# Performance work log

Hardware: AMD Instinct MI355X
Metric: run time of the kernel (lower is better)

## Reference

```python
import jax, jax.numpy as jnp
import numpy as np

N_NODES = 100000
N_EDGES = 1600000
D_IN = 128
D_HID = 128
N_LAYERS = 3


def setup_inputs() -> dict:
    key = jax.random.key(0)
    ks = jax.random.split(key, 7)
    x = jax.random.normal(ks[0], (N_NODES, D_IN), dtype=jnp.float32)
    edge_index = jax.random.randint(ks[1], (2, N_EDGES), 0, N_NODES, dtype=jnp.int32)
    s = 1.0 / np.sqrt(D_HID)
    # stacked per-layer MLP params: lin1 (in->h), lin2 (h->h); in==h==128 for all layers
    W1 = jax.random.uniform(ks[2], (N_LAYERS, D_IN, D_HID), jnp.float32, -s, s)
    b1 = jax.random.uniform(ks[3], (N_LAYERS, D_HID), jnp.float32, -s, s)
    W2 = jax.random.uniform(ks[4], (N_LAYERS, D_HID, D_HID), jnp.float32, -s, s)
    b2 = jax.random.uniform(ks[5], (N_LAYERS, D_HID), jnp.float32, -s, s)
    return {"x": x, "edge_index": edge_index, "W1": W1, "b1": b1, "W2": W2, "b2": b2}


def _gin_layer(x, src, dst, W1, b1, W2, b2):
    # GINConv: out = MLP((1+eps)*x + sum_{j in N(i)} x_j), eps = 0
    agg = jax.ops.segment_sum(x[src], dst, num_segments=N_NODES)  # [N, C]
    h = x + agg
    h = jnp.maximum(h @ W1 + b1, 0.0)  # MLP internal ReLU
    return h @ W2 + b2


def reference(x, edge_index, W1, b1, W2, b2):
    src, dst = edge_index[0], edge_index[1]
    for i in range(N_LAYERS):
        x = _gin_layer(x, src, dst, W1[i], b1[i], W2[i], b2[i])
        if i < N_LAYERS - 1:  # inter-layer act (norm=Identity, dropout=0)
            x = jnp.maximum(x, 0.0)
    return x
```

## Files before the change

### kernel.cpp

```cpp
#include <hip/hip_runtime.h>
#include <hip/hip_bf16.h>

#define D 128

typedef float f32x4 __attribute__((ext_vector_type(4)));
typedef __bf16 bf16x8 __attribute__((ext_vector_type(8)));

__device__ __forceinline__ unsigned short f2bf(float f) {
  unsigned int u = __float_as_uint(f);
  u += 0x7fff + ((u >> 16) & 1);
  return (unsigned short)(u >> 16);
}

__device__ __forceinline__ void gl_lds16(const void* g, void* l) {
  __builtin_amdgcn_global_load_lds(
      (const __attribute__((address_space(1))) unsigned int*)g,
      (__attribute__((address_space(3))) unsigned int*)l, 16, 0, 0);
}


__global__ void k_hist(const int* __restrict__ dst, int E, int* __restrict__ deg) {
  int e = blockIdx.x * 256 + threadIdx.x;
  if (e < E) atomicAdd(&deg[dst[e]], 1);
}

__device__ __forceinline__ int wave_incl_scan(int v, int lane) {
#pragma unroll
  for (int d = 1; d < 64; d <<= 1) {
    int t = __shfl_up(v, d);
    if (lane >= d) v += t;
  }
  return v;
}

__global__ void k_bsum(const int* __restrict__ deg, int N, int* __restrict__ bsum) {
  int i = blockIdx.x * 256 + threadIdx.x;
  int v = (i < N) ? deg[i] : 0;
#pragma unroll
  for (int d = 32; d >= 1; d >>= 1) v += __shfl_down(v, d);
  __shared__ int ws[4];
  if ((threadIdx.x & 63) == 0) ws[threadIdx.x >> 6] = v;
  __syncthreads();
  if (threadIdx.x == 0) bsum[blockIdx.x] = ws[0] + ws[1] + ws[2] + ws[3];
}

__global__ void k_scanp(const int* __restrict__ bsum, int NB, int* __restrict__ bscan,
                        int* __restrict__ total_out) {
  int t = threadIdx.x;
  int lane = t & 63, w = t >> 6;
  int v = (t < NB) ? bsum[t] : 0;
  int s = wave_incl_scan(v, lane);
  __shared__ int ws[8];
  if (lane == 63) ws[w] = s;
  __syncthreads();
  int off = 0;
  for (int i = 0; i < w; i++) off += ws[i];
  if (t < NB) bscan[t] = off + s - v;
  if (t == 0) {
    int tot = 0;
    for (int i = 0; i < 8; i++) tot += ws[i];
    total_out[0] = tot;
  }
}

__global__ void k_scanf(const int* __restrict__ deg, int N, const int* __restrict__ bscan,
                        int* __restrict__ row_ptr) {
  int i = blockIdx.x * 256 + threadIdx.x;
  int lane = threadIdx.x & 63, w = threadIdx.x >> 6;
  int v = (i < N) ? deg[i] : 0;
  int s = wave_incl_scan(v, lane);
  __shared__ int ws[4];
  if (lane == 63) ws[w] = s;
  __syncthreads();
  int off = 0;
  for (int k = 0; k < w; k++) off += ws[k];
  if (i < N) row_ptr[i] = bscan[blockIdx.x] + off + s - v;
}

#define NBK 196
#define CHUNK 4096
__global__ __launch_bounds__(256) void k_binA(const int* __restrict__ src,
                                              const int* __restrict__ dst, int E,
                                              const int* __restrict__ row_ptr,
                                              int* __restrict__ bcursor,
                                              int* __restrict__ pairbuf) {
  __shared__ int cnt[NBK];
  __shared__ int base[NBK];
  const int tid = threadIdx.x;
  const int e0 = blockIdx.x * CHUNK;
  const int emax = min(e0 + CHUNK, E);
  for (int i = tid; i < NBK; i += 256) cnt[i] = 0;
  __syncthreads();
  for (int e = e0 + tid; e < emax; e += 256)
    atomicAdd(&cnt[((unsigned)dst[e]) >> 9], 1);
  __syncthreads();
  for (int i = tid; i < NBK; i += 256) {
    int c = cnt[i];
    int b = 0;
    if (c) b = atomicAdd(&bcursor[i], c) + row_ptr[i << 9];
    base[i] = b;
    cnt[i] = 0;
  }
  __syncthreads();
  for (int e = e0 + tid; e < emax; e += 256) {
    int d = dst[e];
    int bk = ((unsigned)d) >> 9;
    int pos = base[bk] + atomicAdd(&cnt[bk], 1);
    pairbuf[pos] = (src[e] << 9) | (d & 511);
  }
}

#define SEG_CAP 12800
__global__ __launch_bounds__(256) void k_binB(const int* __restrict__ pairbuf,
                                              const int* __restrict__ row_ptr,
                                              int* __restrict__ col, int N) {
  __shared__ int rp[513];
  __shared__ int cur[512];
  __shared__ int stage[SEG_CAP];
  const int tid = threadIdx.x;
  const int node0 = blockIdx.x << 9;
  const int nn = min(512, N - node0);
  for (int i = tid; i <= nn; i += 256) rp[i] = row_ptr[node0 + i];
  for (int i = tid; i < 512; i += 256) cur[i] = 0;
  __syncthreads();
  const int start = rp[0];
  const int sz = rp[nn] - start;
  for (int i = tid; i < sz; i += 256) {
    int pk = pairbuf[start + i];
    int d = pk & 511;
    int pos = (rp[d] - start) + atomicAdd(&cur[d], 1);
    if (pos < SEG_CAP) stage[pos] = (int)(((unsigned)pk) >> 9);
  }
  __syncthreads();
  for (int i = tid; i < sz; i += 256) col[start + i] = stage[i];
}

__global__ __launch_bounds__(256) void k_agg(const unsigned short* __restrict__ Y,
                                             const int* __restrict__ row_ptr,
                                             const int* __restrict__ col,
                                             const float* __restrict__ bias,
                                             unsigned short* __restrict__ H, int N) {
  int wid = (blockIdx.x * 256 + threadIdx.x) >> 6;
  int lane = threadIdx.x & 63;
  if (wid >= N) return;
  const unsigned int* Yu = (const unsigned int*)Y;
  unsigned int sv = Yu[(size_t)wid * 64 + lane];
  float2 bv = ((const float2*)bias)[lane];
  float ax = bv.x + __uint_as_float(sv << 16);
  float ay = bv.y + __uint_as_float(sv & 0xffff0000u);
  int rs = row_ptr[wid], re = row_ptr[wid + 1];
  int deg = re - rs;
  int dcap = min(deg, 64);
  int cv = (lane < dcap) ? col[rs + lane] : 0;
  int j = 0;
  for (; j + 8 <= dcap; j += 8) {
    int s0 = __shfl(cv, j + 0), s1 = __shfl(cv, j + 1);
    int s2 = __shfl(cv, j + 2), s3 = __shfl(cv, j + 3);
    int s4 = __shfl(cv, j + 4), s5 = __shfl(cv, j + 5);
    int s6 = __shfl(cv, j + 6), s7 = __shfl(cv, j + 7);
    unsigned int v0 = Yu[(size_t)s0 * 64 + lane];
    unsigned int v1 = Yu[(size_t)s1 * 64 + lane];
    unsigned int v2 = Yu[(size_t)s2 * 64 + lane];
    unsigned int v3 = Yu[(size_t)s3 * 64 + lane];
    unsigned int v4 = Yu[(size_t)s4 * 64 + lane];
    unsigned int v5 = Yu[(size_t)s5 * 64 + lane];
    unsigned int v6 = Yu[(size_t)s6 * 64 + lane];
    unsigned int v7 = Yu[(size_t)s7 * 64 + lane];
    ax += ((__uint_as_float(v0 << 16) + __uint_as_float(v1 << 16)) +
           (__uint_as_float(v2 << 16) + __uint_as_float(v3 << 16))) +
          ((__uint_as_float(v4 << 16) + __uint_as_float(v5 << 16)) +
           (__uint_as_float(v6 << 16) + __uint_as_float(v7 << 16)));
    ay += ((__uint_as_float(v0 & 0xffff0000u) + __uint_as_float(v1 & 0xffff0000u)) +
           (__uint_as_float(v2 & 0xffff0000u) + __uint_as_float(v3 & 0xffff0000u))) +
          ((__uint_as_float(v4 & 0xffff0000u) + __uint_as_float(v5 & 0xffff0000u)) +
           (__uint_as_float(v6 & 0xffff0000u) + __uint_as_float(v7 & 0xffff0000u)));
  }
  for (; j < dcap; j++) {
    int s = __shfl(cv, j);
    unsigned int v = Yu[(size_t)s * 64 + lane];
    ax += __uint_as_float(v << 16);
    ay += __uint_as_float(v & 0xffff0000u);
  }
  for (int t = rs + 64; t < re; t++) {
    unsigned int v = Yu[(size_t)col[t] * 64 + lane];
    ax += __uint_as_float(v << 16);
    ay += __uint_as_float(v & 0xffff0000u);
  }
  ax = fmaxf(ax, 0.f);
  ay = fmaxf(ay, 0.f);
  unsigned int packed = ((unsigned int)f2bf(ay) << 16) | f2bf(ax);
  ((unsigned int*)H)[(size_t)wid * 64 + lane] = packed;
}

__global__ void k_prep(const float* __restrict__ W1, const float* __restrict__ W2,
                       unsigned short* __restrict__ Wt) {
  int b = blockIdx.x;
  const float* W = (b & 1) ? (W2 + (size_t)(b >> 1) * D * D) : (W1 + (size_t)(b >> 1) * D * D);
  unsigned short* O = Wt + (size_t)b * D * D;
  for (int i = threadIdx.x; i < D * D; i += 256) {
    int n = i >> 7, k = i & 127;
    O[n * D + k] = f2bf(W[k * D + n]);
  }
}

template <bool A_FP32, bool OUT_FP32>
__global__ __launch_bounds__(256) void k_gemm(const void* __restrict__ Ain,
                                              const unsigned short* __restrict__ Wt,
                                              const float* __restrict__ bias,
                                              void* __restrict__ Cout, int M, int relu) {
  __shared__ __align__(16) unsigned short As[64 * 128];
  __shared__ __align__(16) unsigned short Bs[128 * 128];
  const int tid = threadIdx.x;
  const int wid = tid >> 6, lane = tid & 63;
  const int R0 = blockIdx.x * 64;

#pragma unroll
  for (int g = 0; g < 8; g++) {
    int flat = g * 256 + tid;
    int n = flat >> 4, p = flat & 15;
    int l = p ^ (n & 15);
    gl_lds16(Wt + (size_t)n * D + l * 8, &Bs[(size_t)(g * 256 + wid * 64) * 8]);
  }
  if (A_FP32) {
    const float* A = (const float*)Ain;
#pragma unroll
    for (int g = 0; g < 4; g++) {
      int flat = g * 256 + tid;
      int row = flat >> 4, p = flat & 15;
      int l = p ^ (row & 15);
      float4 a0 = make_float4(0.f, 0.f, 0.f, 0.f), a1 = a0;
      if (R0 + row < M) {
        a0 = *(const float4*)(A + (size_t)(R0 + row) * D + l * 8);
        a1 = *(const float4*)(A + (size_t)(R0 + row) * D + l * 8 + 4);
      }
      ushort4 v0, v1;
      v0.x = f2bf(a0.x); v0.y = f2bf(a0.y); v0.z = f2bf(a0.z); v0.w = f2bf(a0.w);
      v1.x = f2bf(a1.x); v1.y = f2bf(a1.y); v1.z = f2bf(a1.z); v1.w = f2bf(a1.w);
      *(ushort4*)&As[row * D + p * 8] = v0;
      *(ushort4*)&As[row * D + p * 8 + 4] = v1;
    }
  } else {
    const unsigned short* A = (const unsigned short*)Ain;
#pragma unroll
    for (int g = 0; g < 4; g++) {
      int flat = g * 256 + tid;
      int row = flat >> 4, p = flat & 15;
      int l = p ^ (row & 15);
      gl_lds16(A + (size_t)(R0 + row) * D + l * 8, &As[(size_t)(g * 256 + wid * 64) * 8]);
    }
  }
  __syncthreads();

  const int wr = wid >> 1, wc = wid & 1;
  const int lm = lane & 15, lq = lane >> 4;
  f32x4 acc[2][4];
#pragma unroll
  for (int i = 0; i < 2; i++)
#pragma unroll
    for (int j = 0; j < 4; j++) acc[i][j] = f32x4{0.f, 0.f, 0.f, 0.f};

#pragma unroll
  for (int kc = 0; kc < 4; kc++) {
    const int pc = (kc * 4 + lq) ^ lm;
    bf16x8 af[2], bfr[4];
#pragma unroll
    for (int i = 0; i < 2; i++)
      af[i] = *(const bf16x8*)&As[(wr * 32 + i * 16 + lm) * D + pc * 8];
#pragma unroll
    for (int j = 0; j < 4; j++)
      bfr[j] = *(const bf16x8*)&Bs[(wc * 64 + j * 16 + lm) * D + pc * 8];
#pragma unroll
    for (int i = 0; i < 2; i++)
#pragma unroll
      for (int j = 0; j < 4; j++)
        acc[i][j] = __builtin_amdgcn_mfma_f32_16x16x32_bf16(af[i], bfr[j], acc[i][j], 0, 0, 0);
  }

  float bv[4];
#pragma unroll
  for (int j = 0; j < 4; j++) bv[j] = bias ? bias[wc * 64 + j * 16 + lm] : 0.f;
#pragma unroll
  for (int i = 0; i < 2; i++) {
#pragma unroll
    for (int reg = 0; reg < 4; reg++) {
      const int gr = R0 + wr * 32 + i * 16 + lq * 4 + reg;
      if (gr < M) {
#pragma unroll
        for (int j = 0; j < 4; j++) {
          const int gc = wc * 64 + j * 16 + lm;
          float v = acc[i][j][reg] + bv[j];
          if (relu) v = fmaxf(v, 0.f);
          if (OUT_FP32)
            ((float*)Cout)[(size_t)gr * D + gc] = v;
          else
            ((unsigned short*)Cout)[(size_t)gr * D + gc] = f2bf(v);
        }
      }
    }
  }
}

extern "C" void kernel_launch(void* const* d_in, const int* in_sizes, int n_in,
                              void* d_out, int out_size, void* d_ws, size_t ws_size,
                              hipStream_t stream) {
  const float* x  = (const float*)d_in[0];
  const int*   ei = (const int*)d_in[1];
  const float* W1 = (const float*)d_in[2];
  const float* b1 = (const float*)d_in[3];
  const float* W2 = (const float*)d_in[4];
  const float* b2 = (const float*)d_in[5];
  const int N = in_sizes[0] / D;
  const int E = in_sizes[1] / 2;
  const int* src = ei;
  const int* dst = ei + E;

  char* ws = (char*)d_ws;
  unsigned short* Wt   = (unsigned short*)ws;
  unsigned short* bufA = Wt + 6 * D * D;
  unsigned short* bufB = bufA + (size_t)N * D;
  int* pairbuf = (int*)bufB;
  int* row_ptr = (int*)(bufB + (size_t)N * D);
  int* deg     = row_ptr + (N + 1);
  int* colv    = deg + N;
  int* bsum    = colv + E;
  int* bscan   = bsum + 1024;
  int* bcursor = bscan + 1024;
  float* OUT   = (float*)d_out;

  const int NB = (N + 255) / 256;
  const int EB = (E + 255) / 256;
  const int GB = (N + 63) / 64;
  const int AB = (N + 3) / 4;
  const int BKB = (N + 511) / 512;

  k_prep<<<6, 256, 0, stream>>>(W1, W2, Wt);
  hipMemsetAsync(deg, 0, (size_t)N * sizeof(int), stream);
  hipMemsetAsync(bcursor, 0, 256 * sizeof(int), stream);
  k_hist<<<EB, 256, 0, stream>>>(dst, E, deg);
  k_bsum<<<NB, 256, 0, stream>>>(deg, N, bsum);
  k_scanp<<<1, 512, 0, stream>>>(bsum, NB, bscan, row_ptr + N);
  k_scanf<<<NB, 256, 0, stream>>>(deg, N, bscan, row_ptr);
  k_binA<<<(E + CHUNK - 1) / CHUNK, 256, 0, stream>>>(src, dst, E, row_ptr, bcursor, pairbuf);
  k_binB<<<BKB, 256, 0, stream>>>(pairbuf, row_ptr, colv, N);

  k_gemm<true, false><<<GB, 256, 0, stream>>>(x, Wt + 0 * D * D, nullptr, bufA, N, 0);
  k_agg<<<AB, 256, 0, stream>>>(bufA, row_ptr, colv, b1, bufB, N);
  k_gemm<false, false><<<GB, 256, 0, stream>>>(bufB, Wt + 1 * D * D, b2, bufA, N, 1);
  k_gemm<false, false><<<GB, 256, 0, stream>>>(bufA, Wt + 2 * D * D, nullptr, bufB, N, 0);
  k_agg<<<AB, 256, 0, stream>>>(bufB, row_ptr, colv, b1 + D, bufA, N);
  k_gemm<false, false><<<GB, 256, 0, stream>>>(bufA, Wt + 3 * D * D, b2 + D, bufB, N, 1);
  k_gemm<false, false><<<GB, 256, 0, stream>>>(bufB, Wt + 4 * D * D, nullptr, bufA, N, 0);
  k_agg<<<AB, 256, 0, stream>>>(bufA, row_ptr, colv, b1 + 2 * D, bufB, N);
  k_gemm<false, true><<<GB, 256, 0, stream>>>(bufB, Wt + 5 * D * D, b2 + 2 * D, OUT, N, 0);
  (void)n_in; (void)out_size; (void)ws_size;
}
```

Before: 502.7 us.

## Build CSR via bucket-level histogram and compute per-node row_ptr inside binning kernel

Replaces the per-node global-atomic degree histogram and three-kernel scan with a per-bucket histogram (LDS-aggregated) and a single small scan over 196 buckets. Per-node degrees and row_ptr are then computed locally inside k_binB using shared-memory atomics and a block scan, eliminating the N-sized memset, 1.6M global atomics, and two full passes over deg. It adds an extra pass over pairbuf in k_binB to count local degrees.

```diff
diff --git a/kernel.cpp b/kernel.cpp
--- a/kernel.cpp
+++ b/kernel.cpp
@@ -18,12 +18,6 @@
       (__attribute__((address_space(3))) unsigned int*)l, 16, 0, 0);
 }
 
-
-__global__ void k_hist(const int* __restrict__ dst, int E, int* __restrict__ deg) {
-  int e = blockIdx.x * 256 + threadIdx.x;
-  if (e < E) atomicAdd(&deg[dst[e]], 1);
-}
-
 __device__ __forceinline__ int wave_incl_scan(int v, int lane) {
 #pragma unroll
   for (int d = 1; d < 64; d <<= 1) {
@@ -33,55 +27,41 @@
   return v;
 }
 
-__global__ void k_bsum(const int* __restrict__ deg, int N, int* __restrict__ bsum) {
-  int i = blockIdx.x * 256 + threadIdx.x;
-  int v = (i < N) ? deg[i] : 0;
-#pragma unroll
-  for (int d = 32; d >= 1; d >>= 1) v += __shfl_down(v, d);
-  __shared__ int ws[4];
-  if ((threadIdx.x & 63) == 0) ws[threadIdx.x >> 6] = v;
-  __syncthreads();
-  if (threadIdx.x == 0) bsum[blockIdx.x] = ws[0] + ws[1] + ws[2] + ws[3];
-}
-
-__global__ void k_scanp(const int* __restrict__ bsum, int NB, int* __restrict__ bscan,
-                        int* __restrict__ total_out) {
+#define NBK 196
+#define CHUNK 4096
+
+__global__ __launch_bounds__(256) void k_bhist(const int* __restrict__ dst, int E,
+                                               int* __restrict__ bcount) {
+  __shared__ int cnt[NBK];
+  const int tid = threadIdx.x;
+  for (int i = tid; i < NBK; i += 256) cnt[i] = 0;
+  __syncthreads();
+  const int e0 = blockIdx.x * CHUNK;
+  const int emax = min(e0 + CHUNK, E);
+  for (int e = e0 + tid; e < emax; e += 256)
+    atomicAdd(&cnt[((unsigned)dst[e]) >> 9], 1);
+  __syncthreads();
+  for (int i = tid; i < NBK; i += 256)
+    if (cnt[i]) atomicAdd(&bcount[i], cnt[i]);
+}
+
+__global__ void k_bscan(const int* __restrict__ bcount, int* __restrict__ bucket_base) {
   int t = threadIdx.x;
   int lane = t & 63, w = t >> 6;
-  int v = (t < NB) ? bsum[t] : 0;
-  int s = wave_incl_scan(v, lane);
-  __shared__ int ws[8];
-  if (lane == 63) ws[w] = s;
-  __syncthreads();
-  int off = 0;
-  for (int i = 0; i < w; i++) off += ws[i];
-  if (t < NB) bscan[t] = off + s - v;
-  if (t == 0) {
-    int tot = 0;
-    for (int i = 0; i < 8; i++) tot += ws[i];
-    total_out[0] = tot;
-  }
-}
-
-__global__ void k_scanf(const int* __restrict__ deg, int N, const int* __restrict__ bscan,
-                        int* __restrict__ row_ptr) {
-  int i = blockIdx.x * 256 + threadIdx.x;
-  int lane = threadIdx.x & 63, w = threadIdx.x >> 6;
-  int v = (i < N) ? deg[i] : 0;
+  int v = (t < NBK) ? bcount[t] : 0;
   int s = wave_incl_scan(v, lane);
   __shared__ int ws[4];
   if (lane == 63) ws[w] = s;
   __syncthreads();
   int off = 0;
-  for (int k = 0; k < w; k++) off += ws[k];
-  if (i < N) row_ptr[i] = bscan[blockIdx.x] + off + s - v;
-}
-
-#define NBK 196
-#define CHUNK 4096
+  for (int i = 0; i < w; i++) off += ws[i];
+  if (t < NBK) bucket_base[t] = off + s - v;
+  if (t == 0) bucket_base[NBK] = ws[0] + ws[1] + ws[2] + ws[3];
+}
+
 __global__ __launch_bounds__(256) void k_binA(const int* __restrict__ src,
                                               const int* __restrict__ dst, int E,
-                                              const int* __restrict__ row_ptr,
+                                              const int* __restrict__ bucket_base,
                                               int* __restrict__ bcursor,
                                               int* __restrict__ pairbuf) {
   __shared__ int cnt[NBK];
@@ -97,7 +77,7 @@
   for (int i = tid; i < NBK; i += 256) {
     int c = cnt[i];
     int b = 0;
-    if (c) b = atomicAdd(&bcursor[i], c) + row_ptr[i << 9];
+    if (c) b = atomicAdd(&bcursor[i], c) + bucket_base[i];
     base[i] = b;
     cnt[i] = 0;
   }
@@ -112,23 +92,43 @@
 
 #define SEG_CAP 12800
 __global__ __launch_bounds__(256) void k_binB(const int* __restrict__ pairbuf,
-                                              const int* __restrict__ row_ptr,
-                                              int* __restrict__ col, int N) {
-  __shared__ int rp[513];
+                                              const int* __restrict__ bucket_base,
+                                              int* __restrict__ col,
+                                              int* __restrict__ row_ptr, int N) {
+  __shared__ int sdeg[512];
+  __shared__ int rpl[512];
   __shared__ int cur[512];
+  __shared__ int wsum[4];
   __shared__ int stage[SEG_CAP];
   const int tid = threadIdx.x;
+  const int lane = tid & 63, wid = tid >> 6;
   const int node0 = blockIdx.x << 9;
   const int nn = min(512, N - node0);
-  for (int i = tid; i <= nn; i += 256) rp[i] = row_ptr[node0 + i];
-  for (int i = tid; i < 512; i += 256) cur[i] = 0;
-  __syncthreads();
-  const int start = rp[0];
-  const int sz = rp[nn] - start;
+  const int start = bucket_base[blockIdx.x];
+  const int end = bucket_base[blockIdx.x + 1];
+  const int sz = end - start;
+  for (int i = tid; i < 512; i += 256) { sdeg[i] = 0; cur[i] = 0; }
+  __syncthreads();
+  for (int i = tid; i < sz; i += 256)
+    atomicAdd(&sdeg[pairbuf[start + i] & 511], 1);
+  __syncthreads();
+  int a = sdeg[2 * tid], b = sdeg[2 * tid + 1];
+  int v = a + b;
+  int s = wave_incl_scan(v, lane);
+  if (lane == 63) wsum[wid] = s;
+  __syncthreads();
+  int off = 0;
+  for (int k = 0; k < wid; k++) off += wsum[k];
+  int e0l = off + s - v;
+  rpl[2 * tid] = e0l;
+  rpl[2 * tid + 1] = e0l + a;
+  __syncthreads();
+  for (int i = tid; i < nn; i += 256) row_ptr[node0 + i] = start + rpl[i];
+  if (blockIdx.x == gridDim.x - 1 && tid == 0) row_ptr[N] = end;
   for (int i = tid; i < sz; i += 256) {
     int pk = pairbuf[start + i];
     int d = pk & 511;
-    int pos = (rp[d] - start) + atomicAdd(&cur[d], 1);
+    int pos = rpl[d] + atomicAdd(&cur[d], 1);
     if (pos < SEG_CAP) stage[pos] = (int)(((unsigned)pk) >> 9);
   }
   __syncthreads();
@@ -320,28 +320,23 @@
   unsigned short* bufB = bufA + (size_t)N * D;
   int* pairbuf = (int*)bufB;
   int* row_ptr = (int*)(bufB + (size_t)N * D);
-  int* deg     = row_ptr + (N + 1);
-  int* colv    = deg + N;
-  int* bsum    = colv + E;
-  int* bscan   = bsum + 1024;
-  int* bcursor = bscan + 1024;
+  int* colv    = row_ptr + (N + 1);
+  int* bucket_base = colv + E;
+  int* bcount  = bucket_base + 256;
+  int* bcursor = bcount + 256;
   float* OUT   = (float*)d_out;
 
-  const int NB = (N + 255) / 256;
-  const int EB = (E + 255) / 256;
+  const int CB = (E + CHUNK - 1) / CHUNK;
   const int GB = (N + 63) / 64;
   const int AB = (N + 3) / 4;
   const int BKB = (N + 511) / 512;
 
   k_prep<<<6, 256, 0, stream>>>(W1, W2, Wt);
-  hipMemsetAsync(deg, 0, (size_t)N * sizeof(int), stream);
-  hipMemsetAsync(bcursor, 0, 256 * sizeof(int), stream);
-  k_hist<<<EB, 256, 0, stream>>>(dst, E, deg);
-  k_bsum<<<NB, 256, 0, stream>>>(deg, N, bsum);
-  k_scanp<<<1, 512, 0, stream>>>(bsum, NB, bscan, row_ptr + N);
-  k_scanf<<<NB, 256, 0, stream>>>(deg, N, bscan, row_ptr);
-  k_binA<<<(E + CHUNK - 1) / CHUNK, 256, 0, stream>>>(src, dst, E, row_ptr, bcursor, pairbuf);
-  k_binB<<<BKB, 256, 0, stream>>>(pairbuf, row_ptr, colv, N);
+  hipMemsetAsync(bcount, 0, 512 * sizeof(int), stream);
+  k_bhist<<<CB, 256, 0, stream>>>(dst, E, bcount);
+  k_bscan<<<1, 256, 0, stream>>>(bcount, bucket_base);
+  k_binA<<<CB, 256, 0, stream>>>(src, dst, E, bucket_base, bcursor, pairbuf);
+  k_binB<<<BKB, 256, 0, stream>>>(pairbuf, bucket_base, colv, row_ptr, N);
 
   k_gemm<true, false><<<GB, 256, 0, stream>>>(x, Wt + 0 * D * D, nullptr, bufA, N, 0);
   k_agg<<<AB, 256, 0, stream>>>(bufA, row_ptr, colv, b1, bufB, N);
```

Result: faster. 447.6 us (-11.0%).
